# Optimization experiments

Hardware: AMD Instinct MI355X
Metric: run time of the kernel (lower is better)

Reference implementation:

```python
import jax, jax.numpy as jnp
import numpy as np

N = 50000        # nodes
E = 800000       # edges
H = 128          # in = hidden = out width
L = 4            # num_layers
BN_EPS = 1e-5


def _bn(x, g, b):
    # training-mode batch norm over the node dimension (biased variance, as torch)
    mu = jnp.mean(x, axis=0)
    var = jnp.mean((x - mu) ** 2, axis=0)
    return (x - mu) * jax.lax.rsqrt(var + BN_EPS) * g + b


def setup_inputs() -> dict:
    key = jax.random.key(0)
    ks = jax.random.split(key, 16)
    s = 0.05
    return {
        "x": jax.random.normal(ks[0], (N, H), dtype=jnp.float32),
        "edge_index": jax.random.randint(ks[1], (2, E), 0, N, dtype=jnp.int32),
        # stacked per-layer MLP params (all layers share dims H->H->H)
        "fc1_w": jax.random.normal(ks[2], (L, H, H), dtype=jnp.float32) * s,
        "fc1_b": jnp.zeros((L, H), dtype=jnp.float32),
        "bn1_g": jnp.ones((L, H), dtype=jnp.float32),
        "bn1_b": jnp.zeros((L, H), dtype=jnp.float32),
        "fc2_w": jax.random.normal(ks[3], (L, H, H), dtype=jnp.float32) * s,
        "fc2_b": jnp.zeros((L, H), dtype=jnp.float32),
        "bn2_g": jnp.ones((L, H), dtype=jnp.float32),
        "bn2_b": jnp.zeros((L, H), dtype=jnp.float32),
        # outer per-layer BatchNorm (intended one-per-GIN-layer)
        "bn3_g": jnp.ones((L, H), dtype=jnp.float32),
        "bn3_b": jnp.zeros((L, H), dtype=jnp.float32),
        # final classifier
        "fc_w": jax.random.normal(ks[4], (H, H), dtype=jnp.float32) * s,
        "fc_b": jnp.zeros((H,), dtype=jnp.float32),
    }


def reference(x, edge_index, fc1_w, fc1_b, bn1_g, bn1_b, fc2_w, fc2_b,
              bn2_g, bn2_b, bn3_g, bn3_b, fc_w, fc_b):
    src = edge_index[0]
    dst = edge_index[1]
    for i in range(L):
        # GINConv, eps=0: h = MLP((1+eps)*x + sum_{j in N(v)} x_j)
        agg = jax.ops.segment_sum(x[src], dst, num_segments=N)  # [N, H]
        h = x + agg
        # MLP: relu(bn1(fc1(h))) -> bn2(fc2(.))
        h = jax.nn.relu(_bn(h @ fc1_w[i].T + fc1_b[i], bn1_g[i], bn1_b[i]))
        h = _bn(h @ fc2_w[i].T + fc2_b[i], bn2_g[i], bn2_b[i])
        # outer BN + ReLU per layer
        x = jax.nn.relu(_bn(h, bn3_g[i], bn3_b[i]))
    return x @ fc_w.T + fc_b  # [N, H]
```

## Files before the change

kernel.cpp:

```cpp
#include <hip/hip_runtime.h>
#include <hip/hip_bf16.h>

#define NN 50000
#define HD 128
#define NL 4
#define BN_EPS 1e-5f
#define NTILES 3125

typedef __attribute__((ext_vector_type(8))) short short8;
typedef __attribute__((ext_vector_type(4))) float f32x4;

__device__ inline ushort f2bf(float f){
  uint u = __float_as_uint(f);
  uint r = (u + 0x7fffu + ((u >> 16) & 1u)) >> 16;
  return (ushort)r;
}
__device__ inline float bflo(uint u){ return __uint_as_float(u << 16); }
__device__ inline float bfhi(uint u){ return __uint_as_float(u & 0xffff0000u); }
__device__ inline uint pk2(float lo, float hi){
  return (uint)f2bf(lo) | ((uint)f2bf(hi) << 16);
}

__global__ void cast_f32_bf16x4(const float* __restrict__ in, ushort* __restrict__ out, int n4){
  int i = blockIdx.x * blockDim.x + threadIdx.x;
  int stride = gridDim.x * blockDim.x;
  const float4* in4 = (const float4*)in;
  for (; i < n4; i += stride){
    float4 v = in4[i];
    ushort4 r;
    r.x = f2bf(v.x); r.y = f2bf(v.y); r.z = f2bf(v.z); r.w = f2bf(v.w);
    *(ushort4*)(out + i * 4) = r;
  }
}

__global__ void cast_weights(const float* __restrict__ w1, const float* __restrict__ w2,
                             const float* __restrict__ wf, ushort* __restrict__ wb){
  int i = blockIdx.x * 256 + threadIdx.x;
  if (i >= 36864) return;
  const float* src;
  if (i < 16384)      src = w1 + i * 4;
  else if (i < 32768) src = w2 + (i - 16384) * 4;
  else                src = wf + (i - 32768) * 4;
  float4 v = *(const float4*)src;
  ushort4 r;
  r.x = f2bf(v.x); r.y = f2bf(v.y); r.z = f2bf(v.z); r.w = f2bf(v.w);
  *(ushort4*)(wb + i * 4) = r;
}

__global__ void fill1_kernel(const int* __restrict__ dst, int* __restrict__ cnt,
                             int* __restrict__ pos, int E){
  int e = (blockIdx.x * 256 + threadIdx.x) * 4;
  if (e + 4 <= E){
    int4 d = *(const int4*)(dst + e);
    int4 p;
    p.x = atomicAdd(&cnt[d.x], 1);
    p.y = atomicAdd(&cnt[d.y], 1);
    p.z = atomicAdd(&cnt[d.z], 1);
    p.w = atomicAdd(&cnt[d.w], 1);
    *(int4*)(pos + e) = p;
  } else {
    for (; e < E; ++e) pos[e] = atomicAdd(&cnt[dst[e]], 1);
  }
}

__global__ void scan1_kernel(const int* __restrict__ deg, int* __restrict__ incl,
                             int* __restrict__ bsum, int n){
  __shared__ int tmp[1024];
  int gid = blockIdx.x * 1024 + threadIdx.x;
  int v = (gid < n) ? deg[gid] : 0;
  tmp[threadIdx.x] = v;
  __syncthreads();
  for (int ofs = 1; ofs < 1024; ofs <<= 1){
    int t = tmp[threadIdx.x];
    int a = (threadIdx.x >= ofs) ? tmp[threadIdx.x - ofs] : 0;
    __syncthreads();
    tmp[threadIdx.x] = t + a;
    __syncthreads();
  }
  if (gid < n) incl[gid] = tmp[threadIdx.x];
  if (threadIdx.x == 1023) bsum[blockIdx.x] = tmp[1023];
}

__global__ void scan2_kernel(const int* __restrict__ bsum, int* __restrict__ base,
                             int* __restrict__ off, int nb, int n){
  int lane = threadIdx.x & 63;
  int own = (lane < nb) ? bsum[lane] : 0;
  int v = own;
#pragma unroll
  for (int ofs = 1; ofs < 64; ofs <<= 1){
    int t = __shfl_up(v, ofs);
    if (lane >= ofs) v += t;
  }
  if (lane < nb) base[lane] = v - own;
  if (lane == 63) off[n] = v;
}

__global__ void scan3_kernel(const int* __restrict__ deg, const int* __restrict__ incl,
                             const int* __restrict__ base, int* __restrict__ off, int n){
  int gid = blockIdx.x * 1024 + threadIdx.x;
  if (gid < n) off[gid] = incl[gid] - deg[gid] + base[blockIdx.x];
}

__global__ void fill2_kernel(const int* __restrict__ src, const int* __restrict__ dst,
                             const int* __restrict__ off, const int* __restrict__ pos,
                             int* __restrict__ csrc, int E){
  int e = (blockIdx.x * 256 + threadIdx.x) * 4;
  if (e + 4 <= E){
    int4 d = *(const int4*)(dst + e);
    int4 p = *(const int4*)(pos + e);
    int4 s = *(const int4*)(src + e);
    csrc[off[d.x] + p.x] = s.x;
    csrc[off[d.y] + p.y] = s.y;
    csrc[off[d.z] + p.z] = s.z;
    csrc[off[d.w] + p.w] = s.w;
  } else {
    for (; e < E; ++e) csrc[off[dst[e]] + pos[e]] = src[e];
  }
}

__device__ inline void bn_params_tid(const float* st, const float* gA, const float* gB,
                                     const float* bB, int mode, float* sS, float* sT){
  int c = threadIdx.x;
  if (c < 128){
    const float invN = 1.f / (float)NN;
    float mu = st[c] * invN;
    float var = fmaxf(st[128 + c] * invN - mu * mu, 0.f);
    float S, T;
    if (mode == 0){
      S = gA[c] * rsqrtf(var + BN_EPS);
      T = gB[c] - mu * S;
    } else {
      float inv2 = rsqrtf(var + BN_EPS);
      float tt = gA[c] * inv2;
      float inv3 = rsqrtf(tt * tt * var + BN_EPS);
      S = tt * inv3 * gB[c];
      T = bB[c] - mu * S;
    }
    sS[c] = S; sT[c] = T;
  }
}

__global__ __launch_bounds__(256) void xform_kernel(const ushort* __restrict__ y,
                                                    const float* __restrict__ statsIn,
                                                    const float* __restrict__ g2,
                                                    const float* __restrict__ g3,
                                                    const float* __restrict__ b3,
                                                    ushort* __restrict__ xo){
  __shared__ float sS[128];
  __shared__ float sT[128];
  bn_params_tid(statsIn, g2, g3, b3, 1, sS, sT);
  __syncthreads();
  int i0 = blockIdx.x * 256 + threadIdx.x;
  int cb = (i0 & 15) * 8;
  float S[8], T[8];
#pragma unroll
  for (int k = 0; k < 8; ++k){ S[k] = sS[cb + k]; T[k] = sT[cb + k]; }
  const uint4* y4 = (const uint4*)y;
  uint4* o4 = (uint4*)xo;
  const int total = NN * 16;
  int stride = gridDim.x * 256;
  for (int i = i0; i < total; i += stride){
    uint4 v = y4[i];
    uint4 r;
    r.x = pk2(fmaxf(bflo(v.x)*S[0]+T[0],0.f), fmaxf(bfhi(v.x)*S[1]+T[1],0.f));
    r.y = pk2(fmaxf(bflo(v.y)*S[2]+T[2],0.f), fmaxf(bfhi(v.y)*S[3]+T[3],0.f));
    r.z = pk2(fmaxf(bflo(v.z)*S[4]+T[4],0.f), fmaxf(bfhi(v.z)*S[5]+T[5],0.f));
    r.w = pk2(fmaxf(bflo(v.w)*S[6]+T[6],0.f), fmaxf(bfhi(v.w)*S[7]+T[7],0.f));
    o4[i] = r;
  }
}

__global__ __launch_bounds__(256) void agg_kernel(const ushort* __restrict__ xb,
                                                  const int* __restrict__ off,
                                                  const int* __restrict__ csrc,
                                                  ushort* __restrict__ h){
  const uint4* x4 = (const uint4*)xb;
  uint4* h4 = (uint4*)h;
  int lane = threadIdx.x & 63;
  int grp  = lane >> 4;
  int col  = lane & 15;
  for (int node = blockIdx.x * 4 + (threadIdx.x >> 6); node < NN; node += gridDim.x * 4){
    int s = off[node], e = off[node + 1];
    float a0, a1, a2, a3, a4, a5, a6, a7;
    if (grp == 0){
      uint4 v = x4[node * 16 + col];
      a0 = bflo(v.x); a1 = bfhi(v.x); a2 = bflo(v.y); a3 = bfhi(v.y);
      a4 = bflo(v.z); a5 = bfhi(v.z); a6 = bflo(v.w); a7 = bfhi(v.w);
    } else {
      a0=0.f;a1=0.f;a2=0.f;a3=0.f;a4=0.f;a5=0.f;a6=0.f;a7=0.f;
    }
    int j = s + grp;
    while (j + 4 < e){
      int r0 = csrc[j];
      int r1 = csrc[j + 4];
      uint4 v0 = x4[r0 * 16 + col];
      uint4 v1 = x4[r1 * 16 + col];
      a0 += bflo(v0.x) + bflo(v1.x); a1 += bfhi(v0.x) + bfhi(v1.x);
      a2 += bflo(v0.y) + bflo(v1.y); a3 += bfhi(v0.y) + bfhi(v1.y);
      a4 += bflo(v0.z) + bflo(v1.z); a5 += bfhi(v0.z) + bfhi(v1.z);
      a6 += bflo(v0.w) + bflo(v1.w); a7 += bfhi(v0.w) + bfhi(v1.w);
      j += 8;
    }
    if (j < e){
      uint4 v = x4[csrc[j] * 16 + col];
      a0 += bflo(v.x); a1 += bfhi(v.x);
      a2 += bflo(v.y); a3 += bfhi(v.y);
      a4 += bflo(v.z); a5 += bfhi(v.z);
      a6 += bflo(v.w); a7 += bfhi(v.w);
    }
    a0 += __shfl_xor(a0, 16); a1 += __shfl_xor(a1, 16);
    a2 += __shfl_xor(a2, 16); a3 += __shfl_xor(a3, 16);
    a4 += __shfl_xor(a4, 16); a5 += __shfl_xor(a5, 16);
    a6 += __shfl_xor(a6, 16); a7 += __shfl_xor(a7, 16);
    a0 += __shfl_xor(a0, 32); a1 += __shfl_xor(a1, 32);
    a2 += __shfl_xor(a2, 32); a3 += __shfl_xor(a3, 32);
    a4 += __shfl_xor(a4, 32); a5 += __shfl_xor(a5, 32);
    a6 += __shfl_xor(a6, 32); a7 += __shfl_xor(a7, 32);
    if (grp == 0){
      uint4 o;
      o.x = pk2(a0, a1); o.y = pk2(a2, a3);
      o.z = pk2(a4, a5); o.w = pk2(a6, a7);
      h4[node * 16 + col] = o;
    }
  }
}

__global__ __launch_bounds__(512) void gemm_kernel(const ushort* __restrict__ A,
                                                   const ushort* __restrict__ W,
                                                   const float* __restrict__ bias,
                                                   ushort* __restrict__ Yb,
                                                   float* __restrict__ Yf,
                                                   float* __restrict__ statsOut,
                                                   const float* __restrict__ statsIn,
                                                   const float* __restrict__ gA,
                                                   const float* __restrict__ gB,
                                                   const float* __restrict__ bB,
                                                   int mode){
  __shared__ uint4 w4[128 * 17];
  __shared__ float ssum[128];
  __shared__ float ssq[128];
  __shared__ float sS[128];
  __shared__ float sT[128];
  const uint4* Wg = (const uint4*)W;
  for (int c = threadIdx.x; c < 2048; c += 512){
    w4[(c >> 4) * 17 + (c & 15)] = Wg[c];
  }
  if (statsIn) bn_params_tid(statsIn, gA, gB, bB, mode, sS, sT);
  if (threadIdx.x < 128){ ssum[threadIdx.x] = 0.f; ssq[threadIdx.x] = 0.f; }
  __syncthreads();

  int wave = threadIdx.x >> 6;
  int lane = threadIdx.x & 63;
  int m = lane & 15, q = lane >> 4;
  int tile = blockIdx.x * 8 + wave;
  bool tv = tile < NTILES;
  const uint4* A4 = (const uint4*)A;

  f32x4 acc[8];
#pragma unroll
  for (int i = 0; i < 8; ++i) acc[i] = (f32x4)0.f;

#pragma unroll
  for (int kt = 0; kt < 4; ++kt){
    short8 af = (short8)0;
    if (tv){
      uint4 t = A4[(tile * 16 + m) * 16 + kt * 4 + q];
      if (statsIn){
        int kc = kt * 32 + q * 8;
        uint4 pk;
        pk.x = (uint)f2bf(fmaxf(bflo(t.x)*sS[kc+0]+sT[kc+0],0.f))
             | ((uint)f2bf(fmaxf(bfhi(t.x)*sS[kc+1]+sT[kc+1],0.f)) << 16);
        pk.y = (uint)f2bf(fmaxf(bflo(t.y)*sS[kc+2]+sT[kc+2],0.f))
             | ((uint)f2bf(fmaxf(bfhi(t.y)*sS[kc+3]+sT[kc+3],0.f)) << 16);
        pk.z = (uint)f2bf(fmaxf(bflo(t.z)*sS[kc+4]+sT[kc+4],0.f))
             | ((uint)f2bf(fmaxf(bfhi(t.z)*sS[kc+5]+sT[kc+5],0.f)) << 16);
        pk.w = (uint)f2bf(fmaxf(bflo(t.w)*sS[kc+6]+sT[kc+6],0.f))
             | ((uint)f2bf(fmaxf(bfhi(t.w)*sS[kc+7]+sT[kc+7],0.f)) << 16);
        t = pk;
      }
      af = *(short8*)&t;
    }
#pragma unroll
    for (int to = 0; to < 8; ++to){
      uint4 bw = w4[(to * 16 + m) * 17 + kt * 4 + q];
      acc[to] = __builtin_amdgcn_mfma_f32_16x16x32_bf16(af, *(short8*)&bw, acc[to], 0, 0, 0);
    }
  }

  bool dost = (statsOut != nullptr);
#pragma unroll
  for (int to = 0; to < 8; ++to){
    int col = to * 16 + m;
    float bc = bias[col];
    float ls = 0.f, lq = 0.f;
    if (tv){
#pragma unroll
      for (int r = 0; r < 4; ++r){
        float v = acc[to][r] + bc;
        int row = tile * 16 + q * 4 + r;
        if (Yb) Yb[row * 128 + col] = __builtin_bit_cast(ushort, f2bf(v));
        else    Yf[row * 128 + col] = v;
        ls += v; lq += v * v;
      }
    }
    if (dost){
      ls += __shfl_xor(ls, 16); lq += __shfl_xor(lq, 16);
      ls += __shfl_xor(ls, 32); lq += __shfl_xor(lq, 32);
      if (tv && q == 0){ atomicAdd(&ssum[col], ls); atomicAdd(&ssq[col], lq); }
    }
  }
  if (dost){
    __syncthreads();
    if (threadIdx.x < 128){
      atomicAdd(&statsOut[threadIdx.x], ssum[threadIdx.x]);
      atomicAdd(&statsOut[128 + threadIdx.x], ssq[threadIdx.x]);
    }
  }
}

extern "C" void kernel_launch(void* const* d_in, const int* in_sizes, int n_in,
                              void* d_out, int out_size, void* d_ws, size_t ws_size,
                              hipStream_t stream) {
  const float* x     = (const float*)d_in[0];
  const int*   ei    = (const int*)d_in[1];
  const float* fc1_w = (const float*)d_in[2];
  const float* fc1_b = (const float*)d_in[3];
  const float* bn1_g = (const float*)d_in[4];
  const float* bn1_b = (const float*)d_in[5];
  const float* fc2_w = (const float*)d_in[6];
  const float* fc2_b = (const float*)d_in[7];
  const float* bn2_g = (const float*)d_in[8];
  const float* bn3_g = (const float*)d_in[10];
  const float* bn3_b = (const float*)d_in[11];
  const float* fc_w  = (const float*)d_in[12];
  const float* fc_b  = (const float*)d_in[13];

  int E = in_sizes[1] / 2;
  const int* srcp = ei;
  const int* dstp = ei + E;

  char* ws = (char*)d_ws;
  int*    off    = (int*)(ws + 0);
  int*    cnt    = (int*)(ws + 200064);
  int*    pos    = (int*)(ws + 400128);
  int*    csrc   = (int*)(ws + 3600128);
  ushort* wb     = (ushort*)(ws + 6800128);
  float*  stats  = (float*)(ws + 7095040);
  int*    sscr   = (int*)(ws + 7103232);
  ushort* xb     = (ushort*)(ws + 7104256);
  ushort* hb     = (ushort*)(ws + 19904256);
  ushort* y1b    = (ushort*)(ws + 32704256);
  ushort* y2b    = (ushort*)(ws + 45504256);

  int* incl = csrc;
  int* bsum = sscr;
  int* base = sscr + 64;

  hipMemsetAsync(cnt, 0, 200064, stream);
  hipMemsetAsync(stats, 0, 8192, stream);

  cast_f32_bf16x4<<<2048, 256, 0, stream>>>(x, xb, NN * HD / 4);
  cast_weights<<<144, 256, 0, stream>>>(fc1_w, fc2_w, fc_w, wb);

  const int EB4 = (E / 4 + 255) / 256 + 1;
  const int SB = (NN + 1023) / 1024;
  fill1_kernel<<<EB4, 256, 0, stream>>>(dstp, cnt, pos, E);
  scan1_kernel<<<SB, 1024, 0, stream>>>(cnt, incl, bsum, NN);
  scan2_kernel<<<1, 64, 0, stream>>>(bsum, base, off, SB, NN);
  scan3_kernel<<<SB, 1024, 0, stream>>>(cnt, incl, base, off, NN);
  fill2_kernel<<<EB4, 256, 0, stream>>>(srcp, dstp, off, pos, csrc, E);

  const int gb = (NTILES + 7) / 8;

  for (int i = 0; i < NL; ++i){
    agg_kernel<<<2048, 256, 0, stream>>>(xb, off, csrc, hb);
    gemm_kernel<<<gb, 512, 0, stream>>>(hb, wb + i * 16384, fc1_b + i * 128,
                                        y1b, nullptr, stats + i * 512,
                                        nullptr, nullptr, nullptr, nullptr, 0);
    gemm_kernel<<<gb, 512, 0, stream>>>(y1b, wb + 65536 + i * 16384, fc2_b + i * 128,
                                        y2b, nullptr, stats + i * 512 + 256,
                                        stats + i * 512, bn1_g + i * 128,
                                        bn1_b + i * 128, nullptr, 0);
    if (i < NL - 1){
      xform_kernel<<<1024, 256, 0, stream>>>(y2b, stats + i * 512 + 256,
                                             bn2_g + i * 128, bn3_g + i * 128,
                                             bn3_b + i * 128, xb);
    }
  }

  gemm_kernel<<<gb, 512, 0, stream>>>(y2b, wb + 131072, fc_b,
                                      nullptr, (float*)d_out, nullptr,
                                      stats + 3 * 512 + 256, bn2_g + 384,
                                      bn3_g + 384, bn3_b + 384, 1);
}
```

Before: 472.1 us.

## Fuse BN transform into aggregation, restructure CSR build, spread stats atomics

Measured after the change: 477.8 us. No clear change (+1.2%).

```diff
diff --git a/kernel.cpp b/kernel.cpp
--- a/kernel.cpp
+++ b/kernel.cpp
@@ -1,5 +1,4 @@
 #include <hip/hip_runtime.h>
-#include <hip/hip_bf16.h>
 
 #define NN 50000
 #define HD 128
@@ -9,6 +8,7 @@
 
 typedef __attribute__((ext_vector_type(8))) short short8;
 typedef __attribute__((ext_vector_type(4))) float f32x4;
+typedef __attribute__((ext_vector_type(4))) uint uint4v;
 
 __device__ inline ushort f2bf(float f){
   uint u = __float_as_uint(f);
@@ -21,45 +21,43 @@
   return (uint)f2bf(lo) | ((uint)f2bf(hi) << 16);
 }
 
-__global__ void cast_f32_bf16x4(const float* __restrict__ in, ushort* __restrict__ out, int n4){
-  int i = blockIdx.x * blockDim.x + threadIdx.x;
-  int stride = gridDim.x * blockDim.x;
-  const float4* in4 = (const float4*)in;
-  for (; i < n4; i += stride){
-    float4 v = in4[i];
+__global__ __launch_bounds__(256) void cast_all(const float* __restrict__ x,
+                                                const float* __restrict__ w1,
+                                                const float* __restrict__ w2,
+                                                const float* __restrict__ wf,
+                                                ushort* __restrict__ xb,
+                                                ushort* __restrict__ wb){
+  const int NX = NN * HD / 4;
+  const int NT = NX + 36864;
+  int i = blockIdx.x * 256 + threadIdx.x;
+  int stride = gridDim.x * 256;
+  for (; i < NT; i += stride){
+    const float* src; ushort* dst;
+    if (i < NX){ src = x + i * 4; dst = xb + i * 4; }
+    else {
+      int k = i - NX;
+      dst = wb + k * 4;
+      if (k < 16384)      src = w1 + k * 4;
+      else if (k < 32768) src = w2 + (k - 16384) * 4;
+      else                src = wf + (k - 32768) * 4;
+    }
+    float4 v = *(const float4*)src;
     ushort4 r;
     r.x = f2bf(v.x); r.y = f2bf(v.y); r.z = f2bf(v.z); r.w = f2bf(v.w);
-    *(ushort4*)(out + i * 4) = r;
-  }
-}
-
-__global__ void cast_weights(const float* __restrict__ w1, const float* __restrict__ w2,
-                             const float* __restrict__ wf, ushort* __restrict__ wb){
-  int i = blockIdx.x * 256 + threadIdx.x;
-  if (i >= 36864) return;
-  const float* src;
-  if (i < 16384)      src = w1 + i * 4;
-  else if (i < 32768) src = w2 + (i - 16384) * 4;
-  else                src = wf + (i - 32768) * 4;
-  float4 v = *(const float4*)src;
-  ushort4 r;
-  r.x = f2bf(v.x); r.y = f2bf(v.y); r.z = f2bf(v.z); r.w = f2bf(v.w);
-  *(ushort4*)(wb + i * 4) = r;
-}
-
-__global__ void fill1_kernel(const int* __restrict__ dst, int* __restrict__ cnt,
-                             int* __restrict__ pos, int E){
+    *(ushort4*)dst = r;
+  }
+}
+
+__global__ void fill1_kernel(const int* __restrict__ dst, int* __restrict__ cnt, int E){
   int e = (blockIdx.x * 256 + threadIdx.x) * 4;
   if (e + 4 <= E){
     int4 d = *(const int4*)(dst + e);
-    int4 p;
-    p.x = atomicAdd(&cnt[d.x], 1);
-    p.y = atomicAdd(&cnt[d.y], 1);
-    p.z = atomicAdd(&cnt[d.z], 1);
-    p.w = atomicAdd(&cnt[d.w], 1);
-    *(int4*)(pos + e) = p;
+    atomicAdd(&cnt[d.x], 1);
+    atomicAdd(&cnt[d.y], 1);
+    atomicAdd(&cnt[d.z], 1);
+    atomicAdd(&cnt[d.w], 1);
   } else {
-    for (; e < E; ++e) pos[e] = atomicAdd(&cnt[dst[e]], 1);
+    for (; e < E; ++e) atomicAdd(&cnt[dst[e]], 1);
   }
 }
 
@@ -96,35 +94,45 @@
 }
 
 __global__ void scan3_kernel(const int* __restrict__ deg, const int* __restrict__ incl,
-                             const int* __restrict__ base, int* __restrict__ off, int n){
+                             const int* __restrict__ base, int* __restrict__ off,
+                             int* __restrict__ cur, int n){
   int gid = blockIdx.x * 1024 + threadIdx.x;
-  if (gid < n) off[gid] = incl[gid] - deg[gid] + base[blockIdx.x];
+  if (gid < n){
+    int o = incl[gid] - deg[gid] + base[blockIdx.x];
+    off[gid] = o;
+    cur[gid] = o;
+  }
 }
 
 __global__ void fill2_kernel(const int* __restrict__ src, const int* __restrict__ dst,
-                             const int* __restrict__ off, const int* __restrict__ pos,
-                             int* __restrict__ csrc, int E){
+                             int* __restrict__ cur, int* __restrict__ csrc, int E){
   int e = (blockIdx.x * 256 + threadIdx.x) * 4;
   if (e + 4 <= E){
     int4 d = *(const int4*)(dst + e);
-    int4 p = *(const int4*)(pos + e);
     int4 s = *(const int4*)(src + e);
-    csrc[off[d.x] + p.x] = s.x;
-    csrc[off[d.y] + p.y] = s.y;
-    csrc[off[d.z] + p.z] = s.z;
-    csrc[off[d.w] + p.w] = s.w;
+    csrc[atomicAdd(&cur[d.x], 1)] = s.x;
+    csrc[atomicAdd(&cur[d.y], 1)] = s.y;
+    csrc[atomicAdd(&cur[d.z], 1)] = s.z;
+    csrc[atomicAdd(&cur[d.w], 1)] = s.w;
   } else {
-    for (; e < E; ++e) csrc[off[dst[e]] + pos[e]] = src[e];
-  }
-}
-
-__device__ inline void bn_params_tid(const float* st, const float* gA, const float* gB,
-                                     const float* bB, int mode, float* sS, float* sT){
+    for (; e < E; ++e) csrc[atomicAdd(&cur[dst[e]], 1)] = src[e];
+  }
+}
+
+__device__ inline void bn_params8(const float* __restrict__ st, const float* __restrict__ gA,
+                                  const float* __restrict__ gB, const float* __restrict__ bB,
+                                  int mode, float* sS, float* sT){
   int c = threadIdx.x;
   if (c < 128){
+    float s0 = 0.f, s1 = 0.f;
+#pragma unroll
+    for (int k = 0; k < 8; ++k){
+      s0 += st[k * 256 + c];
+      s1 += st[k * 256 + 128 + c];
+    }
     const float invN = 1.f / (float)NN;
-    float mu = st[c] * invN;
-    float var = fmaxf(st[128 + c] * invN - mu * mu, 0.f);
+    float mu = s0 * invN;
+    float var = fmaxf(s1 * invN - mu * mu, 0.f);
     float S, T;
     if (mode == 0){
       S = gA[c] * rsqrtf(var + BN_EPS);
@@ -140,89 +148,79 @@
   }
 }
 
-__global__ __launch_bounds__(256) void xform_kernel(const ushort* __restrict__ y,
-                                                    const float* __restrict__ statsIn,
-                                                    const float* __restrict__ g2,
-                                                    const float* __restrict__ g3,
-                                                    const float* __restrict__ b3,
-                                                    ushort* __restrict__ xo){
+template<bool AFF>
+__global__ __launch_bounds__(256) void agg_t(const ushort* __restrict__ xin,
+                                             const int* __restrict__ off,
+                                             const int* __restrict__ csrc,
+                                             const float* __restrict__ statsIn,
+                                             const float* __restrict__ g2,
+                                             const float* __restrict__ g3,
+                                             const float* __restrict__ b3,
+                                             ushort* __restrict__ h){
   __shared__ float sS[128];
   __shared__ float sT[128];
-  bn_params_tid(statsIn, g2, g3, b3, 1, sS, sT);
-  __syncthreads();
-  int i0 = blockIdx.x * 256 + threadIdx.x;
-  int cb = (i0 & 15) * 8;
-  float S[8], T[8];
-#pragma unroll
-  for (int k = 0; k < 8; ++k){ S[k] = sS[cb + k]; T[k] = sT[cb + k]; }
-  const uint4* y4 = (const uint4*)y;
-  uint4* o4 = (uint4*)xo;
-  const int total = NN * 16;
-  int stride = gridDim.x * 256;
-  for (int i = i0; i < total; i += stride){
-    uint4 v = y4[i];
-    uint4 r;
-    r.x = pk2(fmaxf(bflo(v.x)*S[0]+T[0],0.f), fmaxf(bfhi(v.x)*S[1]+T[1],0.f));
-    r.y = pk2(fmaxf(bflo(v.y)*S[2]+T[2],0.f), fmaxf(bfhi(v.y)*S[3]+T[3],0.f));
-    r.z = pk2(fmaxf(bflo(v.z)*S[4]+T[4],0.f), fmaxf(bfhi(v.z)*S[5]+T[5],0.f));
-    r.w = pk2(fmaxf(bflo(v.w)*S[6]+T[6],0.f), fmaxf(bfhi(v.w)*S[7]+T[7],0.f));
-    o4[i] = r;
-  }
-}
-
-__global__ __launch_bounds__(256) void agg_kernel(const ushort* __restrict__ xb,
-                                                  const int* __restrict__ off,
-                                                  const int* __restrict__ csrc,
-                                                  ushort* __restrict__ h){
-  const uint4* x4 = (const uint4*)xb;
-  uint4* h4 = (uint4*)h;
+  if (AFF){
+    bn_params8(statsIn, g2, g3, b3, 1, sS, sT);
+    __syncthreads();
+  }
   int lane = threadIdx.x & 63;
   int grp  = lane >> 4;
   int col  = lane & 15;
-  for (int node = blockIdx.x * 4 + (threadIdx.x >> 6); node < NN; node += gridDim.x * 4){
-    int s = off[node], e = off[node + 1];
-    float a0, a1, a2, a3, a4, a5, a6, a7;
-    if (grp == 0){
-      uint4 v = x4[node * 16 + col];
-      a0 = bflo(v.x); a1 = bfhi(v.x); a2 = bflo(v.y); a3 = bfhi(v.y);
-      a4 = bflo(v.z); a5 = bfhi(v.z); a6 = bflo(v.w); a7 = bfhi(v.w);
+  int node = blockIdx.x * 16 + (threadIdx.x >> 6) * 4 + grp;
+
+  float S[8], T[8];
+  if (AFF){
+#pragma unroll
+    for (int k = 0; k < 8; ++k){ S[k] = sS[col * 8 + k]; T[k] = sT[col * 8 + k]; }
+  }
+
+  const uint4v* x4 = (const uint4v*)xin;
+  int s = off[node], e = off[node + 1];
+
+  float a[8];
+  {
+    uint4v v = x4[node * 16 + col];
+    if (AFF){
+      a[0]=fmaxf(bflo(v.x)*S[0]+T[0],0.f); a[1]=fmaxf(bfhi(v.x)*S[1]+T[1],0.f);
+      a[2]=fmaxf(bflo(v.y)*S[2]+T[2],0.f); a[3]=fmaxf(bfhi(v.y)*S[3]+T[3],0.f);
+      a[4]=fmaxf(bflo(v.z)*S[4]+T[4],0.f); a[5]=fmaxf(bfhi(v.z)*S[5]+T[5],0.f);
+      a[6]=fmaxf(bflo(v.w)*S[6]+T[6],0.f); a[7]=fmaxf(bfhi(v.w)*S[7]+T[7],0.f);
     } else {
-      a0=0.f;a1=0.f;a2=0.f;a3=0.f;a4=0.f;a5=0.f;a6=0.f;a7=0.f;
-    }
-    int j = s + grp;
-    while (j + 4 < e){
-      int r0 = csrc[j];
-      int r1 = csrc[j + 4];
-      uint4 v0 = x4[r0 * 16 + col];
-      uint4 v1 = x4[r1 * 16 + col];
-      a0 += bflo(v0.x) + bflo(v1.x); a1 += bfhi(v0.x) + bfhi(v1.x);
-      a2 += bflo(v0.y) + bflo(v1.y); a3 += bfhi(v0.y) + bfhi(v1.y);
-      a4 += bflo(v0.z) + bflo(v1.z); a5 += bfhi(v0.z) + bfhi(v1.z);
-      a6 += bflo(v0.w) + bflo(v1.w); a7 += bfhi(v0.w) + bfhi(v1.w);
-      j += 8;
-    }
-    if (j < e){
-      uint4 v = x4[csrc[j] * 16 + col];
-      a0 += bflo(v.x); a1 += bfhi(v.x);
-      a2 += bflo(v.y); a3 += bfhi(v.y);
-      a4 += bflo(v.z); a5 += bfhi(v.z);
-      a6 += bflo(v.w); a7 += bfhi(v.w);
-    }
-    a0 += __shfl_xor(a0, 16); a1 += __shfl_xor(a1, 16);
-    a2 += __shfl_xor(a2, 16); a3 += __shfl_xor(a3, 16);
-    a4 += __shfl_xor(a4, 16); a5 += __shfl_xor(a5, 16);
-    a6 += __shfl_xor(a6, 16); a7 += __shfl_xor(a7, 16);
-    a0 += __shfl_xor(a0, 32); a1 += __shfl_xor(a1, 32);
-    a2 += __shfl_xor(a2, 32); a3 += __shfl_xor(a3, 32);
-    a4 += __shfl_xor(a4, 32); a5 += __shfl_xor(a5, 32);
-    a6 += __shfl_xor(a6, 32); a7 += __shfl_xor(a7, 32);
-    if (grp == 0){
-      uint4 o;
-      o.x = pk2(a0, a1); o.y = pk2(a2, a3);
-      o.z = pk2(a4, a5); o.w = pk2(a6, a7);
-      h4[node * 16 + col] = o;
-    }
-  }
+      a[0]=bflo(v.x); a[1]=bfhi(v.x); a[2]=bflo(v.y); a[3]=bfhi(v.y);
+      a[4]=bflo(v.z); a[5]=bfhi(v.z); a[6]=bflo(v.w); a[7]=bfhi(v.w);
+    }
+  }
+
+#define ACC8(v)                                                                 \
+  if (AFF){                                                                     \
+    a[0]+=fmaxf(bflo((v).x)*S[0]+T[0],0.f); a[1]+=fmaxf(bfhi((v).x)*S[1]+T[1],0.f); \
+    a[2]+=fmaxf(bflo((v).y)*S[2]+T[2],0.f); a[3]+=fmaxf(bfhi((v).y)*S[3]+T[3],0.f); \
+    a[4]+=fmaxf(bflo((v).z)*S[4]+T[4],0.f); a[5]+=fmaxf(bfhi((v).z)*S[5]+T[5],0.f); \
+    a[6]+=fmaxf(bflo((v).w)*S[6]+T[6],0.f); a[7]+=fmaxf(bfhi((v).w)*S[7]+T[7],0.f); \
+  } else {                                                                      \
+    a[0]+=bflo((v).x); a[1]+=bfhi((v).x); a[2]+=bflo((v).y); a[3]+=bfhi((v).y); \
+    a[4]+=bflo((v).z); a[5]+=bfhi((v).z); a[6]+=bflo((v).w); a[7]+=bfhi((v).w); \
+  }
+
+  int j = s;
+  for (; j + 4 <= e; j += 4){
+    int i0 = csrc[j], i1 = csrc[j+1], i2 = csrc[j+2], i3 = csrc[j+3];
+    uint4v v0 = x4[i0 * 16 + col];
+    uint4v v1 = x4[i1 * 16 + col];
+    uint4v v2 = x4[i2 * 16 + col];
+    uint4v v3 = x4[i3 * 16 + col];
+    ACC8(v0); ACC8(v1); ACC8(v2); ACC8(v3);
+  }
+  for (; j < e; ++j){
+    uint4v v = x4[csrc[j] * 16 + col];
+    ACC8(v);
+  }
+#undef ACC8
+
+  uint4v o;
+  o.x = pk2(a[0], a[1]); o.y = pk2(a[2], a[3]);
+  o.z = pk2(a[4], a[5]); o.w = pk2(a[6], a[7]);
+  __builtin_nontemporal_store(o, (uint4v*)h + node * 16 + col);
 }
 
 __global__ __launch_bounds__(512) void gemm_kernel(const ushort* __restrict__ A,
@@ -236,16 +234,16 @@
                                                    const float* __restrict__ gB,
                                                    const float* __restrict__ bB,
                                                    int mode){
-  __shared__ uint4 w4[128 * 17];
+  __shared__ uint4v w4[128 * 17];
   __shared__ float ssum[128];
   __shared__ float ssq[128];
   __shared__ float sS[128];
   __shared__ float sT[128];
-  const uint4* Wg = (const uint4*)W;
+  const uint4v* Wg = (const uint4v*)W;
   for (int c = threadIdx.x; c < 2048; c += 512){
     w4[(c >> 4) * 17 + (c & 15)] = Wg[c];
   }
-  if (statsIn) bn_params_tid(statsIn, gA, gB, bB, mode, sS, sT);
+  if (statsIn) bn_params8(statsIn, gA, gB, bB, mode, sS, sT);
   if (threadIdx.x < 128){ ssum[threadIdx.x] = 0.f; ssq[threadIdx.x] = 0.f; }
   __syncthreads();
 
@@ -254,7 +252,7 @@
   int m = lane & 15, q = lane >> 4;
   int tile = blockIdx.x * 8 + wave;
   bool tv = tile < NTILES;
-  const uint4* A4 = (const uint4*)A;
+  const uint4v* A4 = (const uint4v*)A;
 
   f32x4 acc[8];
 #pragma unroll
@@ -264,25 +262,25 @@
   for (int kt = 0; kt < 4; ++kt){
     short8 af = (short8)0;
     if (tv){
-      uint4 t = A4[(tile * 16 + m) * 16 + kt * 4 + q];
+      uint4v t = __builtin_nontemporal_load(A4 + (tile * 16 + m) * 16 + kt * 4 + q);
       if (statsIn){
         int kc = kt * 32 + q * 8;
-        uint4 pk;
-        pk.x = (uint)f2bf(fmaxf(bflo(t.x)*sS[kc+0]+sT[kc+0],0.f))
-             | ((uint)f2bf(fmaxf(bfhi(t.x)*sS[kc+1]+sT[kc+1],0.f)) << 16);
-        pk.y = (uint)f2bf(fmaxf(bflo(t.y)*sS[kc+2]+sT[kc+2],0.f))
-             | ((uint)f2bf(fmaxf(bfhi(t.y)*sS[kc+3]+sT[kc+3],0.f)) << 16);
-        pk.z = (uint)f2bf(fmaxf(bflo(t.z)*sS[kc+4]+sT[kc+4],0.f))
-             | ((uint)f2bf(fmaxf(bfhi(t.z)*sS[kc+5]+sT[kc+5],0.f)) << 16);
-        pk.w = (uint)f2bf(fmaxf(bflo(t.w)*sS[kc+6]+sT[kc+6],0.f))
-             | ((uint)f2bf(fmaxf(bfhi(t.w)*sS[kc+7]+sT[kc+7],0.f)) << 16);
+        uint4v pk;
+        pk.x = pk2(fmaxf(bflo(t.x)*sS[kc+0]+sT[kc+0],0.f),
+                   fmaxf(bfhi(t.x)*sS[kc+1]+sT[kc+1],0.f));
+        pk.y = pk2(fmaxf(bflo(t.y)*sS[kc+2]+sT[kc+2],0.f),
+                   fmaxf(bfhi(t.y)*sS[kc+3]+sT[kc+3],0.f));
+        pk.z = pk2(fmaxf(bflo(t.z)*sS[kc+4]+sT[kc+4],0.f),
+                   fmaxf(bfhi(t.z)*sS[kc+5]+sT[kc+5],0.f));
+        pk.w = pk2(fmaxf(bflo(t.w)*sS[kc+6]+sT[kc+6],0.f),
+                   fmaxf(bfhi(t.w)*sS[kc+7]+sT[kc+7],0.f));
         t = pk;
       }
       af = *(short8*)&t;
     }
 #pragma unroll
     for (int to = 0; to < 8; ++to){
-      uint4 bw = w4[(to * 16 + m) * 17 + kt * 4 + q];
+      uint4v bw = w4[(to * 16 + m) * 17 + kt * 4 + q];
       acc[to] = __builtin_amdgcn_mfma_f32_16x16x32_bf16(af, *(short8*)&bw, acc[to], 0, 0, 0);
     }
   }
@@ -298,8 +296,8 @@
       for (int r = 0; r < 4; ++r){
         float v = acc[to][r] + bc;
         int row = tile * 16 + q * 4 + r;
-        if (Yb) Yb[row * 128 + col] = __builtin_bit_cast(ushort, f2bf(v));
-        else    Yf[row * 128 + col] = v;
+        if (Yb) __builtin_nontemporal_store(__builtin_bit_cast(ushort, f2bf(v)), Yb + row * 128 + col);
+        else    __builtin_nontemporal_store(v, Yf + row * 128 + col);
         ls += v; lq += v * v;
       }
     }
@@ -312,8 +310,9 @@
   if (dost){
     __syncthreads();
     if (threadIdx.x < 128){
-      atomicAdd(&statsOut[threadIdx.x], ssum[threadIdx.x]);
-      atomicAdd(&statsOut[128 + threadIdx.x], ssq[threadIdx.x]);
+      int sb = (blockIdx.x & 7) * 256;
+      atomicAdd(&statsOut[sb + threadIdx.x], ssum[threadIdx.x]);
+      atomicAdd(&statsOut[sb + 128 + threadIdx.x], ssq[threadIdx.x]);
     }
   }
 }
@@ -342,54 +341,57 @@
   char* ws = (char*)d_ws;
   int*    off    = (int*)(ws + 0);
   int*    cnt    = (int*)(ws + 200064);
-  int*    pos    = (int*)(ws + 400128);
-  int*    csrc   = (int*)(ws + 3600128);
-  ushort* wb     = (ushort*)(ws + 6800128);
-  float*  stats  = (float*)(ws + 7095040);
-  int*    sscr   = (int*)(ws + 7103232);
-  ushort* xb     = (ushort*)(ws + 7104256);
-  ushort* hb     = (ushort*)(ws + 19904256);
-  ushort* y1b    = (ushort*)(ws + 32704256);
-  ushort* y2b    = (ushort*)(ws + 45504256);
+  int*    cur    = (int*)(ws + 400128);
+  int*    csrc   = (int*)(ws + 600128);
+  ushort* wb     = (ushort*)(ws + 3800128);
+  float*  stats  = (float*)(ws + 4095040);
+  int*    sscr   = (int*)(ws + 4160576);
+  ushort* xb     = (ushort*)(ws + 4161664);
+  ushort* hb     = (ushort*)(ws + 16961664);
+  ushort* y1b    = (ushort*)(ws + 29761664);
+  ushort* y2b    = (ushort*)(ws + 42561664);
 
   int* incl = csrc;
   int* bsum = sscr;
   int* base = sscr + 64;
 
   hipMemsetAsync(cnt, 0, 200064, stream);
-  hipMemsetAsync(stats, 0, 8192, stream);
-
-  cast_f32_bf16x4<<<2048, 256, 0, stream>>>(x, xb, NN * HD / 4);
-  cast_weights<<<144, 256, 0, stream>>>(fc1_w, fc2_w, fc_w, wb);
+  hipMemsetAsync(stats, 0, 65536, stream);
+
+  cast_all<<<2048, 256, 0, stream>>>(x, fc1_w, fc2_w, fc_w, xb, wb);
 
   const int EB4 = (E / 4 + 255) / 256 + 1;
   const int SB = (NN + 1023) / 1024;
-  fill1_kernel<<<EB4, 256, 0, stream>>>(dstp, cnt, pos, E);
+  fill1_kernel<<<EB4, 256, 0, stream>>>(dstp, cnt, E);
   scan1_kernel<<<SB, 1024, 0, stream>>>(cnt, incl, bsum, NN);
   scan2_kernel<<<1, 64, 0, stream>>>(bsum, base, off, SB, NN);
-  scan3_kernel<<<SB, 1024, 0, stream>>>(cnt, incl, base, off, NN);
-  fill2_kernel<<<EB4, 256, 0, stream>>>(srcp, dstp, off, pos, csrc, E);
+  scan3_kernel<<<SB, 1024, 0, stream>>>(cnt, incl, base, off, cur, NN);
+  fill2_kernel<<<EB4, 256, 0, stream>>>(srcp, dstp, cur, csrc, E);
 
   const int gb = (NTILES + 7) / 8;
 
   for (int i = 0; i < NL; ++i){
-    agg_kernel<<<2048, 256, 0, stream>>>(xb, off, csrc, hb);
+    if (i == 0){
+      agg_t<false><<<NN / 16, 256, 0, stream>>>(xb, off, csrc,
+                                                nullptr, nullptr, nullptr, nullptr, hb);
+    } else {
+      agg_t<true><<<NN / 16, 256, 0, stream>>>(y2b, off, csrc,
+                                               stats + ((i - 1) * 2 + 1) * 2048,
+                                               bn2_g + (i - 1) * 128,
+                                               bn3_g + (i - 1) * 128,
+                                               bn3_b + (i - 1) * 128, hb);
+    }
     gemm_kernel<<<gb, 512, 0, stream>>>(hb, wb + i * 16384, fc1_b + i * 128,
-                                        y1b, nullptr, stats + i * 512,
+                                        y1b, nullptr, stats + (i * 2) * 2048,
                                         nullptr, nullptr, nullptr, nullptr, 0);
     gemm_kernel<<<gb, 512, 0, stream>>>(y1b, wb + 65536 + i * 16384, fc2_b + i * 128,
-                                        y2b, nullptr, stats + i * 512 + 256,
-                                        stats + i * 512, bn1_g + i * 128,
+                                        y2b, nullptr, stats + (i * 2 + 1) * 2048,
+                                        stats + (i * 2) * 2048, bn1_g + i * 128,
                                         bn1_b + i * 128, nullptr, 0);
-    if (i < NL - 1){
-      xform_kernel<<<1024, 256, 0, stream>>>(y2b, stats + i * 512 + 256,
-                                             bn2_g + i * 128, bn3_g + i * 128,
-                                             bn3_b + i * 128, xb);
-    }
   }
 
   gemm_kernel<<<gb, 512, 0, stream>>>(y2b, wb + 131072, fc_b,
                                       nullptr, (float*)d_out, nullptr,
-                                      stats + 3 * 512 + 256, bn2_g + 384,
+                                      stats + 7 * 2048, bn2_g + 384,
                                       bn3_g + 384, bn3_b + 384, 1);
 }
```
